# Optimization experiments

Hardware: AMD Instinct MI355X
Metric: run time of the kernel (lower is better)

The kernel has to match this reference:

```python
import jax, jax.numpy as jnp
import numpy as np

N_NODES = 50000
N_EDGES = 400000
F_IN = 256
HID = 64
N_CLS = 32
HEADS = 8
NEG_SLOPE = 0.2


def setup_inputs() -> dict:
    key = jax.random.key(0)
    ks = jax.random.split(key, 12)
    x = jax.random.normal(ks[0], (N_NODES, F_IN), dtype=jnp.float32)
    edge_index = jax.random.randint(ks[1], (2, N_EDGES), 0, N_NODES, dtype=jnp.int64)

    def glorot(k, shape, fan_in):
        return jax.random.normal(k, shape, dtype=jnp.float32) / np.sqrt(fan_in)

    # layer 1: in=F_IN, heads=HEADS, per-head dim=HID
    Wl1 = glorot(ks[2], (F_IN, HEADS * HID), F_IN)
    Wr1 = glorot(ks[3], (F_IN, HEADS * HID), F_IN)
    att1 = glorot(ks[4], (HEADS, HID), HID)
    b1 = jnp.zeros((HID,), dtype=jnp.float32)
    # layer 2: in=HID, heads=HEADS, per-head dim=N_CLS
    Wl2 = glorot(ks[5], (HID, HEADS * N_CLS), HID)
    Wr2 = glorot(ks[6], (HID, HEADS * N_CLS), HID)
    att2 = glorot(ks[7], (HEADS, N_CLS), N_CLS)
    b2 = jnp.zeros((N_CLS,), dtype=jnp.float32)
    # residual linear
    Wlin = glorot(ks[8], (F_IN, N_CLS), F_IN)
    blin = jnp.zeros((N_CLS,), dtype=jnp.float32)
    return {"x": x, "edge_index": edge_index,
            "Wl1": Wl1, "Wr1": Wr1, "att1": att1, "b1": b1,
            "Wl2": Wl2, "Wr2": Wr2, "att2": att2, "b2": b2,
            "Wlin": Wlin, "blin": blin}


def _gatv2(h, src, dst, Wl, Wr, att, b, n_nodes):
    """GATv2Conv, heads concat=False (head-mean). src/dst: [E] edge endpoints."""
    H, C = att.shape
    xl = (h @ Wl).reshape(n_nodes, H, C)  # source transform
    xr = (h @ Wr).reshape(n_nodes, H, C)  # target transform
    # per-edge attention logit: a . leaky_relu(x_l[src] + x_r[dst])
    e = jax.nn.leaky_relu(xl[src] + xr[dst], NEG_SLOPE)  # [E, H, C]
    logits = jnp.einsum('ehc,hc->eh', e, att)            # [E, H]
    # segment softmax over incoming edges of each target node
    m = jax.ops.segment_max(logits, dst, num_segments=n_nodes)
    m = jnp.where(jnp.isfinite(m), m, 0.0)
    p = jnp.exp(logits - m[dst])
    denom = jax.ops.segment_sum(p, dst, num_segments=n_nodes)
    alpha = p / denom[dst]                               # [E, H]
    out = jax.ops.segment_sum(xl[src] * alpha[:, :, None], dst,
                              num_segments=n_nodes)      # [N, H, C]
    return out.mean(axis=1) + b


def reference(x, edge_index, Wl1, Wr1, att1, b1, Wl2, Wr2, att2, b2, Wlin, blin):
    n = x.shape[0]
    # PyG GATv2Conv default add_self_loops=True
    loops = jnp.arange(n, dtype=edge_index.dtype)
    src = jnp.concatenate([edge_index[0], loops])
    dst = jnp.concatenate([edge_index[1], loops])
    residual = x @ Wlin + blin
    h = jax.nn.relu(_gatv2(x, src, dst, Wl1, Wr1, att1, b1, n))
    # dropout(p=0.25) is identity in eval mode
    out = _gatv2(h, src, dst, Wl2, Wr2, att2, b2, n)
    return out + residual
```

## Files before the change

### kernel.cpp

```cpp
#include <hip/hip_runtime.h>
#include <cmath>


#define NEG_SLOPE 0.2f

typedef __attribute__((ext_vector_type(4))) float f32x4;
typedef __attribute__((ext_vector_type(8))) short bf16x8;

__device__ inline unsigned short f2b(float f) {
    union { float f; unsigned u; } c; c.f = f;
    return (unsigned short)((c.u + 0x8000u) >> 16);
}
__device__ inline float b2f_lo(unsigned u) { union { unsigned i; float f; } c; c.i = u << 16; return c.f; }
__device__ inline float b2f_hi(unsigned u) { union { unsigned i; float f; } c; c.i = u & 0xffff0000u; return c.f; }

__device__ inline void cstore(float* C, size_t i, float v) { C[i] = v; }
__device__ inline void cstore(unsigned short* C, size_t i, float v) { C[i] = f2b(v); }

__device__ inline void store4(unsigned short* C, size_t idx, f32x4 v) {
    uint2 pk;
    pk.x = f2b(v[0]) | ((unsigned)f2b(v[1]) << 16);
    pk.y = f2b(v[2]) | ((unsigned)f2b(v[3]) << 16);
    *(uint2*)(C + idx) = pk;
}
__device__ inline void store4(float* C, size_t idx, f32x4 v) {
    *(f32x4*)(C + idx) = v;
}

__device__ inline void gl_lds16(const void* g, void* l) {
    __builtin_amdgcn_global_load_lds(
        (const __attribute__((address_space(1))) void*)g,
        (__attribute__((address_space(3))) void*)l, 16, 0, 0);
}

__device__ inline int swz(int c) { return (c & ~7) | ((c ^ (c >> 3)) & 7); }

template <int VPL> struct RawV;
template <> struct RawV<8> { uint4 v; };
template <> struct RawV<4> { uint2 v; };

template <int VPL>
__device__ inline RawV<VPL> load_raw(const unsigned short* __restrict__ p) {
    RawV<VPL> r;
    if constexpr (VPL == 8) r.v = *reinterpret_cast<const uint4*>(p);
    else                    r.v = *reinterpret_cast<const uint2*>(p);
    return r;
}
template <int VPL>
__device__ inline void conv_raw(const RawV<VPL>& r, float* v) {
    if constexpr (VPL == 8) {
        unsigned u[4] = {r.v.x, r.v.y, r.v.z, r.v.w};
#pragma unroll
        for (int i = 0; i < 4; i++) { v[2 * i] = b2f_lo(u[i]); v[2 * i + 1] = b2f_hi(u[i]); }
    } else {
        unsigned u[2] = {r.v.x, r.v.y};
#pragma unroll
        for (int i = 0; i < 2; i++) { v[2 * i] = b2f_lo(u[i]); v[2 * i + 1] = b2f_hi(u[i]); }
    }
}

__global__ void k_zero(int* __restrict__ p, int n) {
    int i = blockIdx.x * blockDim.x + threadIdx.x;
    if (i < n) p[i] = 0;
}

__global__ void k_conv_x(const float* __restrict__ x, unsigned short* __restrict__ xb,
                         int n_elems, int total_elems) {
    int i = (blockIdx.x * blockDim.x + threadIdx.x) * 8;
    if (i >= total_elems) return;
    uint4 pk;
    if (i < n_elems) {
        float4 f0 = *(const float4*)(x + i);
        float4 f1 = *(const float4*)(x + i + 4);
        pk.x = f2b(f0.x) | ((unsigned)f2b(f0.y) << 16);
        pk.y = f2b(f0.z) | ((unsigned)f2b(f0.w) << 16);
        pk.z = f2b(f1.x) | ((unsigned)f2b(f1.y) << 16);
        pk.w = f2b(f1.z) | ((unsigned)f2b(f1.w) << 16);
    } else {
        pk = uint4{0, 0, 0, 0};
    }
    *(uint4*)(xb + i) = pk;
}

__global__ void k_edge_deg(const int* __restrict__ ei, int* __restrict__ deg,
                           int E, int ET) {
    int e = blockIdx.x * blockDim.x + threadIdx.x;
    if (e >= ET) return;
    int dst = (e < E) ? ei[E + e] : (e - E);
    atomicAdd(&deg[dst], 1);
}
__global__ void k_scan1(const int* __restrict__ deg, int* __restrict__ offs,
                        int* __restrict__ sums, int n) {
    __shared__ int tmp[256];
    int tid = threadIdx.x;
    int i = blockIdx.x * 256 + tid;
    int v = (i < n) ? deg[i] : 0;
    tmp[tid] = v;
    __syncthreads();
    for (int ofs = 1; ofs < 256; ofs <<= 1) {
        int add = (tid >= ofs) ? tmp[tid - ofs] : 0;
        __syncthreads();
        tmp[tid] += add;
        __syncthreads();
    }
    if (i < n) offs[i] = tmp[tid] - v;
    if (tid == 255) sums[blockIdx.x] = tmp[255];
}
__global__ void k_scan2(int* __restrict__ sums, int nb) {
    __shared__ int tmp[256];
    int tid = threadIdx.x;
    int v = (tid < nb) ? sums[tid] : 0;
    tmp[tid] = v;
    __syncthreads();
    for (int ofs = 1; ofs < 256; ofs <<= 1) {
        int add = (tid >= ofs) ? tmp[tid - ofs] : 0;
        __syncthreads();
        tmp[tid] += add;
        __syncthreads();
    }
    if (tid < nb) sums[tid] = tmp[tid] - v;
}
__global__ void k_scan3(int* __restrict__ offs, int* __restrict__ cursor,
                        const int* __restrict__ sums, int n, int total) {
    int i = blockIdx.x * blockDim.x + threadIdx.x;
    if (i < n) {
        int v = offs[i] + sums[i >> 8];
        offs[i] = v;
        cursor[i] = v;
    }
    if (i == 0) offs[n] = total;
}
__global__ void k_edge_scatter(const int* __restrict__ ei, int* __restrict__ cursor,
                               int* __restrict__ csr_src, int E, int ET) {
    int e = blockIdx.x * blockDim.x + threadIdx.x;
    if (e >= ET) return;
    int src, dst;
    if (e < E) { src = ei[e]; dst = ei[E + e]; }
    else { src = dst = e - E; }
    int pos = atomicAdd(&cursor[dst], 1);
    csr_src[pos] = src;
}

__global__ void k_conv_w(const float* __restrict__ Wl1, const float* __restrict__ Wr1,
                         const float* __restrict__ Wl2, const float* __restrict__ Wr2,
                         const float* __restrict__ Wlin,
                         unsigned short* __restrict__ Wlr1t,
                         unsigned short* __restrict__ Wlr2t,
                         unsigned short* __restrict__ WlinT) {
    int i = blockIdx.x * blockDim.x + threadIdx.x;
    if (i < 1024 * 256) {
        int n = i >> 8, k = i & 255;
        float v = (n < 512) ? Wl1[k * 512 + n] : Wr1[k * 512 + (n - 512)];
        Wlr1t[i] = f2b(v);
        return;
    }
    i -= 1024 * 256;
    if (i < 512 * 64) {
        int n = i >> 6, k = i & 63;
        float v = (n < 256) ? Wl2[k * 256 + n] : Wr2[k * 256 + (n - 256)];
        Wlr2t[i] = f2b(v);
        return;
    }
    i -= 512 * 64;
    if (i < 128 * 256) {
        int n = i >> 8, k = i & 255;
        WlinT[i] = (n < 32) ? f2b(Wlin[k * 32 + n]) : (unsigned short)0;
    }
}

template <typename CT>
__device__ inline void mfma_body(const unsigned short* __restrict__ A,
                                 const unsigned short* __restrict__ Bt,
                                 const float* __restrict__ bias,
                                 CT* __restrict__ C1, CT* __restrict__ C2, int csplit,
                                 int Mreal, int Mout, int Nc, int K,
                                 int mt, int gx, int bid,
                                 unsigned short* As, unsigned short* Bs) {
    int xcd = bid & 7, j = bid >> 3;
    int rpx = (mt + 7) >> 3;
    int row_t = xcd * rpx + j / gx;
    int col_t = j % gx;
    if (row_t >= mt) return;
    int row0 = row_t * 128, col0 = col_t * 128;

    int tid = threadIdx.x;
    int lane = tid & 63, wid = tid >> 6;
    int wm = (wid & 1) * 64, wn = (wid >> 1) * 64;
    f32x4 acc[4][4] = {};

    for (int k0 = 0; k0 < K; k0 += 64) {
#pragma unroll
        for (int it = 0; it < 4; it++) {
            int p = tid + it * 256;
            int l = swz(p);
            int r = l >> 3, kc = (l & 7) * 8;
            int gr = row0 + r; if (gr > Mreal - 1) gr = Mreal - 1;
            gl_lds16(A + (size_t)gr * K + k0 + kc, &As[p * 8]);
            gl_lds16(Bt + (size_t)(col0 + r) * K + k0 + kc, &Bs[p * 8]);
        }
        __syncthreads();
#pragma unroll
        for (int kh = 0; kh < 2; kh++) {
            bf16x8 af[4], bfv[4];
#pragma unroll
            for (int mi = 0; mi < 4; mi++) {
                int l = (wm + mi * 16 + (lane & 15)) * 8 + kh * 4 + (lane >> 4);
                af[mi] = *(const bf16x8*)&As[swz(l) * 8];
            }
#pragma unroll
            for (int ni = 0; ni < 4; ni++) {
                int l = (wn + ni * 16 + (lane & 15)) * 8 + kh * 4 + (lane >> 4);
                bfv[ni] = *(const bf16x8*)&Bs[swz(l) * 8];
            }
#pragma unroll
            for (int mi = 0; mi < 4; mi++)
#pragma unroll
                for (int ni = 0; ni < 4; ni++)
                    acc[mi][ni] = __builtin_amdgcn_mfma_f32_16x16x32_bf16(
                        bfv[ni], af[mi], acc[mi][ni], 0, 0, 0);
        }
        __syncthreads();
    }
    CT* Cb; int cstride, cbase;
    if (col0 < csplit) { Cb = C1; cstride = csplit;      cbase = 0; }
    else               { Cb = C2; cstride = Nc - csplit; cbase = csplit; }
    int crow = lane & 15, cquad = (lane >> 4) * 4;
#pragma unroll
    for (int mi = 0; mi < 4; mi++) {
        int grow = row0 + wm + mi * 16 + crow;
        if (grow >= Mout) continue;
#pragma unroll
        for (int ni = 0; ni < 4; ni++) {
            int gcol = col0 + wn + ni * 16 + cquad;
            if (gcol >= Nc) continue;
            f32x4 v = acc[mi][ni];
            if (bias) {
                float4 bv = *(const float4*)(bias + gcol);
                v[0] += bv.x; v[1] += bv.y; v[2] += bv.z; v[3] += bv.w;
            }
            store4(Cb, (size_t)grow * cstride + (gcol - cbase), v);
        }
    }
}

template <typename CT>
__global__ __launch_bounds__(256)
void k_mfma(const unsigned short* __restrict__ A, const unsigned short* __restrict__ Bt,
            const float* __restrict__ bias, CT* __restrict__ C1, CT* __restrict__ C2,
            int csplit, int Mreal, int Mout, int Nc, int K, int mt, int gx) {
    alignas(16) __shared__ unsigned short As[128 * 64];
    alignas(16) __shared__ unsigned short Bs[128 * 64];
    mfma_body<CT>(A, Bt, bias, C1, C2, csplit, Mreal, Mout, Nc, K, mt, gx,
                  blockIdx.x, As, Bs);
}

__global__ __launch_bounds__(256)
void k_mfma_dual(const unsigned short* __restrict__ A1, const unsigned short* __restrict__ B1,
                 unsigned short* __restrict__ xl2, unsigned short* __restrict__ xr2,
                 const unsigned short* __restrict__ A2, const unsigned short* __restrict__ B2,
                 const float* __restrict__ bias2, float* __restrict__ C2,
                 int N, int Mp, int mt, int split) {
    alignas(16) __shared__ unsigned short As[128 * 64];
    alignas(16) __shared__ unsigned short Bs[128 * 64];
    int bid = blockIdx.x;
    if (bid < split)
        mfma_body<unsigned short>(A1, B1, nullptr, xl2, xr2, 256, N, N, 512, 64,
                                  mt, 4, bid, As, Bs);
    else
        mfma_body<float>(A2, B2, bias2, C2, C2, 32, Mp, N, 32, 256,
                         mt, 1, bid - split, As, Bs);
}

template <int C, bool RELU_OUT, bool ADD_RES, typename OutT>
__global__ void k_agg(const unsigned short* __restrict__ xl,
                      const unsigned short* __restrict__ xr,
                      const float* __restrict__ att, const float* __restrict__ bias,
                      const float* __restrict__ res,
                      const int* __restrict__ offs, const int* __restrict__ csr_src,
                      OutT* __restrict__ out, int n_nodes) {
    constexpr int H = 8;
    constexpr int D = H * C;
    constexpr int VPL = D / 64;
    int wave = (blockIdx.x * blockDim.x + threadIdx.x) >> 6;
    int lane = threadIdx.x & 63;
    if (wave >= n_nodes) return;
    int n = wave;
    int base = lane * VPL;
    const unsigned short* bp = xl + base;

    float xr_n[VPL], att_l[VPL], acc[VPL];
    {
        RawV<VPL> rr = load_raw<VPL>(xr + (size_t)n * D + base);
        conv_raw<VPL>(rr, xr_n);
    }
#pragma unroll
    for (int j = 0; j < VPL; j++) { att_l[j] = att[base + j]; acc[j] = 0.f; }

    float lsum = 0.f;
    int e0 = offs[n], e1 = offs[n + 1], last = e1 - 1;
#define GADDR(t) (bp + (size_t)csr_src[min(t, last)] * D)
    RawV<VPL> r0 = load_raw<VPL>(GADDR(e0));
    RawV<VPL> r1 = load_raw<VPL>(GADDR(e0 + 1));
    RawV<VPL> r2 = load_raw<VPL>(GADDR(e0 + 2));
    RawV<VPL> r3 = load_raw<VPL>(GADDR(e0 + 3));

    auto step = [&](const float* xsv) {
        float partial = 0.f;
#pragma unroll
        for (int j = 0; j < VPL; j++) {
            float v = xsv[j] + xr_n[j];
            float lr = fmaxf(v, NEG_SLOPE * v);
            partial += att_l[j] * lr;
        }
        partial += __shfl_xor(partial, 1);
        partial += __shfl_xor(partial, 2);
        partial += __shfl_xor(partial, 4);
        float p = __expf(partial);
        lsum += p;
#pragma unroll
        for (int j = 0; j < VPL; j++) acc[j] += p * xsv[j];
    };

    for (int e = e0; e < e1; e += 4) {
        float xsv[VPL];
        conv_raw<VPL>(r0, xsv); r0 = load_raw<VPL>(GADDR(e + 4));
        step(xsv);
        conv_raw<VPL>(r1, xsv); r1 = load_raw<VPL>(GADDR(e + 5));
        if (e + 1 < e1) step(xsv);
        conv_raw<VPL>(r2, xsv); r2 = load_raw<VPL>(GADDR(e + 6));
        if (e + 2 < e1) step(xsv);
        conv_raw<VPL>(r3, xsv); r3 = load_raw<VPL>(GADDR(e + 7));
        if (e + 3 < e1) step(xsv);
    }
#undef GADDR
    float inv = 1.f / lsum;
#pragma unroll
    for (int j = 0; j < VPL; j++) acc[j] *= inv;
#pragma unroll
    for (int j = 0; j < VPL; j++) {
        acc[j] += __shfl_xor(acc[j], 8);
        acc[j] += __shfl_xor(acc[j], 16);
        acc[j] += __shfl_xor(acc[j], 32);
    }
    if (lane < 8) {
#pragma unroll
        for (int j = 0; j < VPL; j++) {
            int c = lane * VPL + j;
            float v = acc[j] * 0.125f + bias[c];
            if (ADD_RES) v += res[(size_t)n * C + c];
            if (RELU_OUT) v = fmaxf(v, 0.f);
            cstore(out, (size_t)n * C + c, v);
        }
    }
}

extern "C" void kernel_launch(void* const* d_in, const int* in_sizes, int n_in,
                              void* d_out, int out_size, void* d_ws, size_t ws_size,
                              hipStream_t stream) {
    const float* x    = (const float*)d_in[0];
    const int* ei     = (const int*)d_in[1];
    const float* Wl1  = (const float*)d_in[2];
    const float* Wr1  = (const float*)d_in[3];
    const float* att1 = (const float*)d_in[4];
    const float* b1   = (const float*)d_in[5];
    const float* Wl2  = (const float*)d_in[6];
    const float* Wr2  = (const float*)d_in[7];
    const float* att2 = (const float*)d_in[8];
    const float* b2   = (const float*)d_in[9];
    const float* Wlin = (const float*)d_in[10];
    const float* blin = (const float*)d_in[11];
    float* out = (float*)d_out;

    const int N  = in_sizes[0] / 256;
    const int E  = in_sizes[1] / 2;
    const int ET = E + N;
    const int Mp = ((N + 127) / 128) * 128;

    size_t need = (size_t)Mp * 1024 * 2 + (size_t)Mp * 256 * 2 + (size_t)Mp * 64 * 2
                + 1024 * 256 * 2 + 512 * 64 * 2 + 128 * 256 * 2
                + (size_t)(N + 1) * 4 + (size_t)N * 4 + (size_t)ET * 4 + 256 * 4 + 256;
    if (ws_size < need) return;

    char* w = (char*)d_ws;
    unsigned short* xl1   = (unsigned short*)w; w += (size_t)Mp * 512 * 2;
    unsigned short* xr1   = (unsigned short*)w; w += (size_t)Mp * 512 * 2;
    unsigned short* xb    = (unsigned short*)w; w += (size_t)Mp * 256 * 2;
    unsigned short* h1    = (unsigned short*)w; w += (size_t)Mp * 64 * 2;
    unsigned short* Wlr1t = (unsigned short*)w; w += 1024 * 256 * 2;
    unsigned short* Wlr2t = (unsigned short*)w; w += 512 * 64 * 2;
    unsigned short* WlinT = (unsigned short*)w; w += 128 * 256 * 2;
    int* offs   = (int*)w; w += (size_t)(N + 1) * 4;
    int* cursor = (int*)w; w += (size_t)N * 4;
    int* csr    = (int*)w; w += (size_t)ET * 4;
    int* sums   = (int*)w; w += 256 * 4;
    unsigned short* xl2 = xl1;
    unsigned short* xr2 = xl1 + (size_t)Mp * 256;
    float* resid = (float*)xr1;

    int nb = (N + 255) / 256;
    k_zero<<<nb, 256, 0, stream>>>(cursor, N);
    k_edge_deg<<<(ET + 255) / 256, 256, 0, stream>>>(ei, cursor, E, ET);
    k_scan1<<<nb, 256, 0, stream>>>(cursor, offs, sums, N);
    k_scan2<<<1, 256, 0, stream>>>(sums, nb);
    k_scan3<<<nb, 256, 0, stream>>>(offs, cursor, sums, N, ET);
    k_edge_scatter<<<(ET + 255) / 256, 256, 0, stream>>>(ei, cursor, csr, E, ET);
    int tot = Mp * 256;
    k_conv_x<<<(tot / 8 + 255) / 256, 256, 0, stream>>>(x, xb, N * 256, tot);
    k_conv_w<<<(1024 * 256 + 512 * 64 + 128 * 256) / 256, 256, 0, stream>>>(
        Wl1, Wr1, Wl2, Wr2, Wlin, Wlr1t, Wlr2t, WlinT);

    int mt = Mp / 128;
    int rpx = (mt + 7) / 8;
    k_mfma<unsigned short><<<8 * rpx * 8, 256, 0, stream>>>(
        xb, Wlr1t, nullptr, xl1, xr1, 512, Mp, N, 1024, 256, mt, 8);
    k_agg<64, true, false><<<(N + 3) / 4, 256, 0, stream>>>(
        xl1, xr1, att1, b1, nullptr, offs, csr, h1, N);
    int split = 8 * rpx * 4;
    k_mfma_dual<<<split + 8 * rpx, 256, 0, stream>>>(
        h1, Wlr2t, xl2, xr2, xb, WlinT, blin, resid, N, Mp, mt, split);
    k_agg<32, false, true><<<(N + 3) / 4, 256, 0, stream>>>(
        xl2, xr2, att2, b2, resid, offs, csr, out, N);
}
```

Before: 379.6 us.

## Merge independent kernels into multi-role launches and pack aggregation math as float2

Fuses the x and weight conversions into one launch. The CSR edge scatter now runs inside the layer-1 GEMM launch, and the residual GEMM runs inside the layer-1 aggregation launch, using block-index role splitting. These cut launch count and let independent work fill idle CUs. The aggregation loop is rewritten with float2 vectors and a remainder tail in place of per-edge predicates. The residual gets its own workspace buffer because it now runs concurrently with reads of xr1. Risk: GEMM blocks sharing a launch with memory-bound agg or atomic blocks may reduce occupancy.

```diff
diff --git a/kernel.cpp b/kernel.cpp
--- a/kernel.cpp
+++ b/kernel.cpp
@@ -5,6 +5,7 @@
 #define NEG_SLOPE 0.2f
 
 typedef __attribute__((ext_vector_type(4))) float f32x4;
+typedef __attribute__((ext_vector_type(2))) float f32x2;
 typedef __attribute__((ext_vector_type(8))) short bf16x8;
 
 __device__ inline unsigned short f2b(float f) {
@@ -47,39 +48,18 @@
     return r;
 }
 template <int VPL>
-__device__ inline void conv_raw(const RawV<VPL>& r, float* v) {
-    if constexpr (VPL == 8) {
-        unsigned u[4] = {r.v.x, r.v.y, r.v.z, r.v.w};
-#pragma unroll
-        for (int i = 0; i < 4; i++) { v[2 * i] = b2f_lo(u[i]); v[2 * i + 1] = b2f_hi(u[i]); }
-    } else {
-        unsigned u[2] = {r.v.x, r.v.y};
-#pragma unroll
-        for (int i = 0; i < 2; i++) { v[2 * i] = b2f_lo(u[i]); v[2 * i + 1] = b2f_hi(u[i]); }
+__device__ inline void conv2(const RawV<VPL>& r, f32x2* v) {
+    const unsigned* u = (const unsigned*)&r.v;
+#pragma unroll
+    for (int i = 0; i < VPL / 2; i++) {
+        f32x2 t; t.x = b2f_lo(u[i]); t.y = b2f_hi(u[i]);
+        v[i] = t;
     }
 }
 
 __global__ void k_zero(int* __restrict__ p, int n) {
     int i = blockIdx.x * blockDim.x + threadIdx.x;
     if (i < n) p[i] = 0;
-}
-
-__global__ void k_conv_x(const float* __restrict__ x, unsigned short* __restrict__ xb,
-                         int n_elems, int total_elems) {
-    int i = (blockIdx.x * blockDim.x + threadIdx.x) * 8;
-    if (i >= total_elems) return;
-    uint4 pk;
-    if (i < n_elems) {
-        float4 f0 = *(const float4*)(x + i);
-        float4 f1 = *(const float4*)(x + i + 4);
-        pk.x = f2b(f0.x) | ((unsigned)f2b(f0.y) << 16);
-        pk.y = f2b(f0.z) | ((unsigned)f2b(f0.w) << 16);
-        pk.z = f2b(f1.x) | ((unsigned)f2b(f1.y) << 16);
-        pk.w = f2b(f1.z) | ((unsigned)f2b(f1.w) << 16);
-    } else {
-        pk = uint4{0, 0, 0, 0};
-    }
-    *(uint4*)(xb + i) = pk;
 }
 
 __global__ void k_edge_deg(const int* __restrict__ ei, int* __restrict__ deg,
@@ -130,24 +110,32 @@
     }
     if (i == 0) offs[n] = total;
 }
-__global__ void k_edge_scatter(const int* __restrict__ ei, int* __restrict__ cursor,
-                               int* __restrict__ csr_src, int E, int ET) {
-    int e = blockIdx.x * blockDim.x + threadIdx.x;
-    if (e >= ET) return;
-    int src, dst;
-    if (e < E) { src = ei[e]; dst = ei[E + e]; }
-    else { src = dst = e - E; }
-    int pos = atomicAdd(&cursor[dst], 1);
-    csr_src[pos] = src;
-}
-
-__global__ void k_conv_w(const float* __restrict__ Wl1, const float* __restrict__ Wr1,
-                         const float* __restrict__ Wl2, const float* __restrict__ Wr2,
-                         const float* __restrict__ Wlin,
-                         unsigned short* __restrict__ Wlr1t,
-                         unsigned short* __restrict__ Wlr2t,
-                         unsigned short* __restrict__ WlinT) {
-    int i = blockIdx.x * blockDim.x + threadIdx.x;
+
+__global__ void k_conv_xw(const float* __restrict__ x, unsigned short* __restrict__ xb,
+                          int n_elems, int xblocks,
+                          const float* __restrict__ Wl1, const float* __restrict__ Wr1,
+                          const float* __restrict__ Wl2, const float* __restrict__ Wr2,
+                          const float* __restrict__ Wlin,
+                          unsigned short* __restrict__ Wlr1t,
+                          unsigned short* __restrict__ Wlr2t,
+                          unsigned short* __restrict__ WlinT) {
+    if ((int)blockIdx.x < xblocks) {
+        int i = (blockIdx.x * 256 + threadIdx.x) * 8;
+        uint4 pk;
+        if (i < n_elems) {
+            float4 f0 = *(const float4*)(x + i);
+            float4 f1 = *(const float4*)(x + i + 4);
+            pk.x = f2b(f0.x) | ((unsigned)f2b(f0.y) << 16);
+            pk.y = f2b(f0.z) | ((unsigned)f2b(f0.w) << 16);
+            pk.z = f2b(f1.x) | ((unsigned)f2b(f1.y) << 16);
+            pk.w = f2b(f1.z) | ((unsigned)f2b(f1.w) << 16);
+        } else {
+            pk = uint4{0, 0, 0, 0};
+        }
+        *(uint4*)(xb + i) = pk;
+        return;
+    }
+    int i = (blockIdx.x - xblocks) * 256 + threadIdx.x;
     if (i < 1024 * 256) {
         int n = i >> 8, k = i & 255;
         float v = (n < 512) ? Wl1[k * 512 + n] : Wr1[k * 512 + (n - 512)];
@@ -243,99 +231,83 @@
     }
 }
 
-template <typename CT>
-__global__ __launch_bounds__(256)
-void k_mfma(const unsigned short* __restrict__ A, const unsigned short* __restrict__ Bt,
-            const float* __restrict__ bias, CT* __restrict__ C1, CT* __restrict__ C2,
-            int csplit, int Mreal, int Mout, int Nc, int K, int mt, int gx) {
-    alignas(16) __shared__ unsigned short As[128 * 64];
-    alignas(16) __shared__ unsigned short Bs[128 * 64];
-    mfma_body<CT>(A, Bt, bias, C1, C2, csplit, Mreal, Mout, Nc, K, mt, gx,
-                  blockIdx.x, As, Bs);
-}
-
-__global__ __launch_bounds__(256)
-void k_mfma_dual(const unsigned short* __restrict__ A1, const unsigned short* __restrict__ B1,
-                 unsigned short* __restrict__ xl2, unsigned short* __restrict__ xr2,
-                 const unsigned short* __restrict__ A2, const unsigned short* __restrict__ B2,
-                 const float* __restrict__ bias2, float* __restrict__ C2,
-                 int N, int Mp, int mt, int split) {
-    alignas(16) __shared__ unsigned short As[128 * 64];
-    alignas(16) __shared__ unsigned short Bs[128 * 64];
-    int bid = blockIdx.x;
-    if (bid < split)
-        mfma_body<unsigned short>(A1, B1, nullptr, xl2, xr2, 256, N, N, 512, 64,
-                                  mt, 4, bid, As, Bs);
-    else
-        mfma_body<float>(A2, B2, bias2, C2, C2, 32, Mp, N, 32, 256,
-                         mt, 1, bid - split, As, Bs);
-}
-
 template <int C, bool RELU_OUT, bool ADD_RES, typename OutT>
-__global__ void k_agg(const unsigned short* __restrict__ xl,
-                      const unsigned short* __restrict__ xr,
-                      const float* __restrict__ att, const float* __restrict__ bias,
-                      const float* __restrict__ res,
-                      const int* __restrict__ offs, const int* __restrict__ csr_src,
-                      OutT* __restrict__ out, int n_nodes) {
-    constexpr int H = 8;
-    constexpr int D = H * C;
+__device__ inline void agg_body(const unsigned short* __restrict__ xl,
+                                const unsigned short* __restrict__ xr,
+                                const float* __restrict__ att, const float* __restrict__ bias,
+                                const float* __restrict__ res,
+                                const int* __restrict__ offs, const int* __restrict__ csr_src,
+                                OutT* __restrict__ out, int n) {
+    constexpr int D = 8 * C;
     constexpr int VPL = D / 64;
-    int wave = (blockIdx.x * blockDim.x + threadIdx.x) >> 6;
+    constexpr int VP2 = VPL / 2;
     int lane = threadIdx.x & 63;
-    if (wave >= n_nodes) return;
-    int n = wave;
     int base = lane * VPL;
     const unsigned short* bp = xl + base;
 
-    float xr_n[VPL], att_l[VPL], acc[VPL];
+    f32x2 xr2[VP2], at2[VP2], ac2[VP2];
     {
         RawV<VPL> rr = load_raw<VPL>(xr + (size_t)n * D + base);
-        conv_raw<VPL>(rr, xr_n);
-    }
-#pragma unroll
-    for (int j = 0; j < VPL; j++) { att_l[j] = att[base + j]; acc[j] = 0.f; }
-
+        conv2<VPL>(rr, xr2);
+    }
+    f32x2 zero2 = {0.f, 0.f};
+#pragma unroll
+    for (int j = 0; j < VP2; j++) {
+        f32x2 a; a.x = att[base + 2 * j]; a.y = att[base + 2 * j + 1];
+        at2[j] = a;
+        ac2[j] = zero2;
+    }
     float lsum = 0.f;
-    int e0 = offs[n], e1 = offs[n + 1], last = e1 - 1;
+    int e0 = offs[n], e1 = offs[n + 1];
+    int deg = e1 - e0, last = e1 - 1;
 #define GADDR(t) (bp + (size_t)csr_src[min(t, last)] * D)
-    RawV<VPL> r0 = load_raw<VPL>(GADDR(e0));
+    RawV<VPL> r0 = load_raw<VPL>(bp + (size_t)csr_src[e0] * D);
     RawV<VPL> r1 = load_raw<VPL>(GADDR(e0 + 1));
     RawV<VPL> r2 = load_raw<VPL>(GADDR(e0 + 2));
     RawV<VPL> r3 = load_raw<VPL>(GADDR(e0 + 3));
 
-    auto step = [&](const float* xsv) {
-        float partial = 0.f;
-#pragma unroll
-        for (int j = 0; j < VPL; j++) {
-            float v = xsv[j] + xr_n[j];
-            float lr = fmaxf(v, NEG_SLOPE * v);
-            partial += att_l[j] * lr;
-        }
+    auto proc = [&](const RawV<VPL>& r) {
+        f32x2 xs2[VP2];
+        conv2<VPL>(r, xs2);
+        f32x2 part2 = zero2;
+#pragma unroll
+        for (int j = 0; j < VP2; j++) {
+            f32x2 v = xs2[j] + xr2[j];
+            f32x2 t = v * NEG_SLOPE;
+            f32x2 lr; lr.x = fmaxf(v.x, t.x); lr.y = fmaxf(v.y, t.y);
+            part2 += at2[j] * lr;
+        }
+        float partial = part2.x + part2.y;
         partial += __shfl_xor(partial, 1);
         partial += __shfl_xor(partial, 2);
         partial += __shfl_xor(partial, 4);
         float p = __expf(partial);
         lsum += p;
-#pragma unroll
-        for (int j = 0; j < VPL; j++) acc[j] += p * xsv[j];
+        f32x2 p2 = {p, p};
+#pragma unroll
+        for (int j = 0; j < VP2; j++) ac2[j] += p2 * xs2[j];
     };
 
-    for (int e = e0; e < e1; e += 4) {
-        float xsv[VPL];
-        conv_raw<VPL>(r0, xsv); r0 = load_raw<VPL>(GADDR(e + 4));
-        step(xsv);
-        conv_raw<VPL>(r1, xsv); r1 = load_raw<VPL>(GADDR(e + 5));
-        if (e + 1 < e1) step(xsv);
-        conv_raw<VPL>(r2, xsv); r2 = load_raw<VPL>(GADDR(e + 6));
-        if (e + 2 < e1) step(xsv);
-        conv_raw<VPL>(r3, xsv); r3 = load_raw<VPL>(GADDR(e + 7));
-        if (e + 3 < e1) step(xsv);
-    }
+    int q = deg >> 2, rem = deg & 3;
+    int e = e0;
+    for (int it = 0; it < q; it++, e += 4) {
+        proc(r0); r0 = load_raw<VPL>(GADDR(e + 4));
+        proc(r1); r1 = load_raw<VPL>(GADDR(e + 5));
+        proc(r2); r2 = load_raw<VPL>(GADDR(e + 6));
+        proc(r3); r3 = load_raw<VPL>(GADDR(e + 7));
+    }
+    if (rem > 0) proc(r0);
+    if (rem > 1) proc(r1);
+    if (rem > 2) proc(r2);
 #undef GADDR
+
     float inv = 1.f / lsum;
-#pragma unroll
-    for (int j = 0; j < VPL; j++) acc[j] *= inv;
+    float acc[VPL];
+#pragma unroll
+    for (int j = 0; j < VP2; j++) {
+        acc[2 * j]     = ac2[j].x * inv;
+        acc[2 * j + 1] = ac2[j].y * inv;
+    }
 #pragma unroll
     for (int j = 0; j < VPL; j++) {
         acc[j] += __shfl_xor(acc[j], 8);
@@ -352,6 +324,71 @@
             cstore(out, (size_t)n * C + c, v);
         }
     }
+}
+
+__global__ __launch_bounds__(256)
+void k_gemm1_scatter(const unsigned short* __restrict__ xb,
+                     const unsigned short* __restrict__ Wlr1t,
+                     unsigned short* __restrict__ xl1, unsigned short* __restrict__ xr1,
+                     const int* __restrict__ ei, int* __restrict__ cursor,
+                     int* __restrict__ csr, int E, int ET,
+                     int N, int Mp, int mt, int gb) {
+    alignas(16) __shared__ unsigned short As[128 * 64];
+    alignas(16) __shared__ unsigned short Bs[128 * 64];
+    int bid = blockIdx.x;
+    if (bid < gb) {
+        mfma_body<unsigned short>(xb, Wlr1t, nullptr, xl1, xr1, 512,
+                                  Mp, N, 1024, 256, mt, 8, bid, As, Bs);
+        return;
+    }
+    int e = (bid - gb) * 256 + threadIdx.x;
+    if (e >= ET) return;
+    int src, dst;
+    if (e < E) { src = ei[e]; dst = ei[E + e]; }
+    else { src = dst = e - E; }
+    int pos = atomicAdd(&cursor[dst], 1);
+    csr[pos] = src;
+}
+
+__global__ __launch_bounds__(256)
+void k_agg1_resid(const unsigned short* __restrict__ xl1, const unsigned short* __restrict__ xr1,
+                  const float* __restrict__ att1, const float* __restrict__ b1,
+                  const int* __restrict__ offs, const int* __restrict__ csr,
+                  unsigned short* __restrict__ h1,
+                  const unsigned short* __restrict__ xb, const unsigned short* __restrict__ WlinT,
+                  const float* __restrict__ blin, float* __restrict__ resid,
+                  int N, int Mp, int mt, int gb) {
+    alignas(16) __shared__ unsigned short As[128 * 64];
+    alignas(16) __shared__ unsigned short Bs[128 * 64];
+    int bid = blockIdx.x;
+    if (bid < gb) {
+        mfma_body<float>(xb, WlinT, blin, resid, resid, 32,
+                         Mp, N, 32, 256, mt, 1, bid, As, Bs);
+        return;
+    }
+    int node = (bid - gb) * 4 + (threadIdx.x >> 6);
+    if (node < N)
+        agg_body<64, true, false>(xl1, xr1, att1, b1, nullptr, offs, csr, h1, node);
+}
+
+__global__ __launch_bounds__(256)
+void k_mfma2(const unsigned short* __restrict__ h1, const unsigned short* __restrict__ Wlr2t,
+             unsigned short* __restrict__ xl2, unsigned short* __restrict__ xr2,
+             int N, int mt) {
+    alignas(16) __shared__ unsigned short As[128 * 64];
+    alignas(16) __shared__ unsigned short Bs[128 * 64];
+    mfma_body<unsigned short>(h1, Wlr2t, nullptr, xl2, xr2, 256,
+                              N, N, 512, 64, mt, 4, blockIdx.x, As, Bs);
+}
+
+__global__ void k_agg2(const unsigned short* __restrict__ xl2, const unsigned short* __restrict__ xr2,
+                       const float* __restrict__ att2, const float* __restrict__ b2,
+                       const float* __restrict__ resid,
+                       const int* __restrict__ offs, const int* __restrict__ csr,
+                       float* __restrict__ out, int N) {
+    int node = (blockIdx.x * blockDim.x + threadIdx.x) >> 6;
+    if (node < N)
+        agg_body<32, false, true>(xl2, xr2, att2, b2, resid, offs, csr, out, node);
 }
 
 extern "C" void kernel_launch(void* const* d_in, const int* in_sizes, int n_in,
@@ -377,6 +414,7 @@
     const int Mp = ((N + 127) / 128) * 128;
 
     size_t need = (size_t)Mp * 1024 * 2 + (size_t)Mp * 256 * 2 + (size_t)Mp * 64 * 2
+                + (size_t)Mp * 32 * 4
                 + 1024 * 256 * 2 + 512 * 64 * 2 + 128 * 256 * 2
                 + (size_t)(N + 1) * 4 + (size_t)N * 4 + (size_t)ET * 4 + 256 * 4 + 256;
     if (ws_size < need) return;
@@ -386,6 +424,7 @@
     unsigned short* xr1   = (unsigned short*)w; w += (size_t)Mp * 512 * 2;
     unsigned short* xb    = (unsigned short*)w; w += (size_t)Mp * 256 * 2;
     unsigned short* h1    = (unsigned short*)w; w += (size_t)Mp * 64 * 2;
+    float* resid          = (float*)w;          w += (size_t)Mp * 32 * 4;
     unsigned short* Wlr1t = (unsigned short*)w; w += 1024 * 256 * 2;
     unsigned short* Wlr2t = (unsigned short*)w; w += 512 * 64 * 2;
     unsigned short* WlinT = (unsigned short*)w; w += 128 * 256 * 2;
@@ -395,7 +434,6 @@
     int* sums   = (int*)w; w += 256 * 4;
     unsigned short* xl2 = xl1;
     unsigned short* xr2 = xl1 + (size_t)Mp * 256;
-    float* resid = (float*)xr1;
 
     int nb = (N + 255) / 256;
     k_zero<<<nb, 256, 0, stream>>>(cursor, N);
@@ -403,21 +441,21 @@
     k_scan1<<<nb, 256, 0, stream>>>(cursor, offs, sums, N);
     k_scan2<<<1, 256, 0, stream>>>(sums, nb);
     k_scan3<<<nb, 256, 0, stream>>>(offs, cursor, sums, N, ET);
-    k_edge_scatter<<<(ET + 255) / 256, 256, 0, stream>>>(ei, cursor, csr, E, ET);
-    int tot = Mp * 256;
-    k_conv_x<<<(tot / 8 + 255) / 256, 256, 0, stream>>>(x, xb, N * 256, tot);
-    k_conv_w<<<(1024 * 256 + 512 * 64 + 128 * 256) / 256, 256, 0, stream>>>(
-        Wl1, Wr1, Wl2, Wr2, Wlin, Wlr1t, Wlr2t, WlinT);
+    int xblocks = (Mp * 256 / 8) / 256;
+    int wblocks = (1024 * 256 + 512 * 64 + 128 * 256 + 255) / 256;
+    k_conv_xw<<<xblocks + wblocks, 256, 0, stream>>>(
+        x, xb, N * 256, xblocks, Wl1, Wr1, Wl2, Wr2, Wlin, Wlr1t, Wlr2t, WlinT);
 
     int mt = Mp / 128;
     int rpx = (mt + 7) / 8;
-    k_mfma<unsigned short><<<8 * rpx * 8, 256, 0, stream>>>(
-        xb, Wlr1t, nullptr, xl1, xr1, 512, Mp, N, 1024, 256, mt, 8);
-    k_agg<64, true, false><<<(N + 3) / 4, 256, 0, stream>>>(
-        xl1, xr1, att1, b1, nullptr, offs, csr, h1, N);
-    int split = 8 * rpx * 4;
-    k_mfma_dual<<<split + 8 * rpx, 256, 0, stream>>>(
-        h1, Wlr2t, xl2, xr2, xb, WlinT, blin, resid, N, Mp, mt, split);
-    k_agg<32, false, true><<<(N + 3) / 4, 256, 0, stream>>>(
-        xl2, xr2, att2, b2, resid, offs, csr, out, N);
-}
+    int gb1 = 8 * rpx * 8;
+    int sb  = (ET + 255) / 256;
+    k_gemm1_scatter<<<gb1 + sb, 256, 0, stream>>>(
+        xb, Wlr1t, xl1, xr1, ei, cursor, csr, E, ET, N, Mp, mt, gb1);
+    int gbr = 8 * rpx;
+    int ab  = (N + 3) / 4;
+    k_agg1_resid<<<gbr + ab, 256, 0, stream>>>(
+        xl1, xr1, att1, b1, offs, csr, h1, xb, WlinT, blin, resid, N, Mp, mt, gbr);
+    k_mfma2<<<8 * rpx * 4, 256, 0, stream>>>(h1, Wlr2t, xl2, xr2, N, mt);
+    k_agg2<<<ab, 256, 0, stream>>>(xl2, xr2, att2, b2, resid, offs, csr, out, N);
+}
```

Measured after the change: 369.3 us. -2.7%, faster.
